# Performance work log

Measured on AMD Instinct MI355X. Metric: run time of the kernel, lower is better.

The kernel has to match this reference:

```python
import jax, jax.numpy as jnp
import numpy as np

N_NODES = 10000
N_EDGES = 320000
IN_FEATS = 512
N_UNITS = 256
OUT_FEATS = 64
N_LAYERS = 6  # number of hidden GCNConv layers feeding the JK max


def setup_inputs() -> dict:
    key = jax.random.key(0)
    ks = jax.random.split(key, 8)
    h = jax.random.normal(ks[0], (N_NODES, IN_FEATS), dtype=jnp.float32)
    edge_index = jax.random.randint(ks[1], (2, N_EDGES), 0, N_NODES, dtype=jnp.int64)
    # learned parameters (glorot-ish scale)
    W0 = jax.random.normal(ks[2], (IN_FEATS, N_UNITS), dtype=jnp.float32) * (1.0 / np.sqrt(IN_FEATS))
    b0 = jnp.zeros((N_UNITS,), dtype=jnp.float32)
    Wh = jax.random.normal(ks[3], (N_LAYERS - 1, N_UNITS, N_UNITS), dtype=jnp.float32) * (1.0 / np.sqrt(N_UNITS))
    bh = jnp.zeros((N_LAYERS - 1, N_UNITS), dtype=jnp.float32)
    Wo = jax.random.normal(ks[4], (N_UNITS, OUT_FEATS), dtype=jnp.float32) * (1.0 / np.sqrt(N_UNITS))
    bo = jnp.zeros((OUT_FEATS,), dtype=jnp.float32)
    return {"h": h, "edge_index": edge_index, "W0": W0, "b0": b0,
            "Wh": Wh, "bh": bh, "Wo": Wo, "bo": bo}


def reference(h, edge_index, W0, b0, Wh, bh, Wo, bo):
    src = edge_index[0]
    dst = edge_index[1]
    n = h.shape[0]

    def conv_plain(x, W, b):
        # GCNConv with normalize=False: plain sum aggregation over edges, no self-loops
        m = x @ W                                   # [N, d]
        agg = jax.ops.segment_sum(m[src], dst, num_segments=n)
        return jax.nn.relu(agg + b)

    outs = []
    x = conv_plain(h, W0, b0)
    outs.append(x)
    for i in range(Wh.shape[0]):  # dropout is identity in eval mode
        x = conv_plain(x, Wh[i], bh[i])
        outs.append(x)

    # jumping-knowledge max aggregation over layer outputs
    x = jnp.max(jnp.stack(outs, axis=0), axis=0)    # [N, n_units]

    # final GCNConv with normalize=True (symmetric GCN norm, self-loops added)
    m = x @ Wo                                      # [N, out_feats]
    ones = jnp.ones(dst.shape, dtype=m.dtype)
    deg = jax.ops.segment_sum(ones, dst, num_segments=n) + 1.0  # +1 self loop
    dinv = deg ** -0.5
    coef = dinv[src] * dinv[dst]                    # [E]
    agg = jax.ops.segment_sum(m[src] * coef[:, None], dst, num_segments=n)
    agg = agg + m / deg[:, None] + bo               # self-loop term 1/deg_i
    return jax.nn.log_softmax(agg, axis=-1)
```

## Files before the change

### kernel.cpp

```cpp
#include <hip/hip_runtime.h>
#include <math.h>

#define N_NODES 10000
#define N_EDGES 320000
#define IN_FEATS 512
#define N_UNITS 256
#define OUT_FEATS 64
#define N_HID 5

typedef __attribute__((ext_vector_type(8))) short bf16x8;
typedef __attribute__((ext_vector_type(4))) float f32x4;

__device__ __forceinline__ unsigned short f2bf(float f) {
    union { float f; unsigned int u; } c; c.f = f;
    unsigned int u = c.u + 0x7FFFu + ((c.u >> 16) & 1u);
    return (unsigned short)(u >> 16);
}
__device__ __forceinline__ float bf2f(unsigned int b) {
    union { unsigned int u; float f; } c; c.u = (b & 0xffffu) << 16;
    return c.f;
}


__global__ void k_setup(const int* __restrict__ dst, int* __restrict__ deg,
                        const float* __restrict__ h, unsigned short* __restrict__ hb,
                        const float* __restrict__ W0, const float* __restrict__ Wh,
                        const float* __restrict__ Wo,
                        unsigned short* __restrict__ W0t, unsigned short* __restrict__ Wht,
                        unsigned short* __restrict__ Wot) {
    const int R1 = N_EDGES;
    const int R2 = N_NODES * IN_FEATS / 4;
    const int S0 = IN_FEATS * N_UNITS;
    const int SH = N_HID * N_UNITS * N_UNITS;
    const int SO = N_UNITS * OUT_FEATS;
    int t = blockIdx.x * blockDim.x + threadIdx.x;
    if (t < R1) {
        atomicAdd(&deg[dst[t]], 1);
    } else if (t < R1 + R2) {
        int u = t - R1;
        float4 v = reinterpret_cast<const float4*>(h)[u];
        ushort4 o;
        o.x = f2bf(v.x); o.y = f2bf(v.y); o.z = f2bf(v.z); o.w = f2bf(v.w);
        reinterpret_cast<ushort4*>(hb)[u] = o;
    } else {
        int u = t - R1 - R2;
        if (u < S0) {
            int k = u >> 8, n = u & 255;
            W0t[(size_t)n * IN_FEATS + k] = f2bf(W0[u]);
        } else if (u < S0 + SH) {
            int w = u - S0;
            int l = w >> 16;
            int r = w & 65535;
            int k = r >> 8, n = r & 255;
            Wht[(size_t)l * 65536 + (size_t)n * N_UNITS + k] = f2bf(Wh[w]);
        } else if (u < S0 + SH + SO) {
            int w = u - S0 - SH;
            int k = w >> 6, n = w & 63;
            Wot[(size_t)n * N_UNITS + k] = f2bf(Wo[w]);
        }
    }
}


__global__ __launch_bounds__(1024) void k_scan(const int* __restrict__ deg,
                                               int* __restrict__ row_ptr,
                                               int* __restrict__ cursor,
                                               float* __restrict__ dinv,
                                               float* __restrict__ invdeg) {
    __shared__ int wsum[16];
    const int PER = 10;
    int t = threadIdx.x;
    int lane = t & 63, wid = t >> 6;
    int base = t * PER;

    int v[PER];
    int s = 0;
#pragma unroll
    for (int j = 0; j < PER; ++j) {
        int i = base + j;
        int d = (i < N_NODES) ? deg[i] : 0;
        v[j] = s;
        s += d;
    }
    int inc = s;
#pragma unroll
    for (int off = 1; off < 64; off <<= 1) {
        int y = __shfl_up(inc, off);
        if (lane >= off) inc += y;
    }
    if (lane == 63) wsum[wid] = inc;
    __syncthreads();
    if (wid == 0) {
        int w = (lane < 16) ? wsum[lane] : 0;
#pragma unroll
        for (int off = 1; off < 16; off <<= 1) {
            int y = __shfl_up(w, off);
            if (lane >= off) w += y;
        }
        if (lane < 16) wsum[lane] = w;
    }
    __syncthreads();
    int wave_excl = (wid == 0) ? 0 : wsum[wid - 1];
    int thread_excl = wave_excl + (inc - s);

#pragma unroll
    for (int j = 0; j < PER; ++j) {
        int i = base + j;
        if (i < N_NODES) {
            int rp = thread_excl + v[j];
            row_ptr[i] = rp;
            cursor[i]  = rp;
            int d = ((j + 1 < PER) ? v[j + 1] : s) - v[j];
            float dd = (float)(d + 1);
            dinv[i]   = rsqrtf(dd);
            invdeg[i] = 1.0f / dd;
        }
    }
    if (t == 1023) row_ptr[N_NODES] = thread_excl + s;
}

__global__ void k_fill(const int* __restrict__ src, const int* __restrict__ dst,
                       int* __restrict__ cursor, int* __restrict__ csr_src) {
    int e = blockIdx.x * blockDim.x + threadIdx.x;
    if (e < N_EDGES) {
        int p = atomicAdd(&cursor[dst[e]], 1);
        csr_src[p] = src[e];
    }
}


__global__ __launch_bounds__(256) void k_mgemm(const unsigned short* __restrict__ A,
                                               const unsigned short* __restrict__ Bt,
                                               unsigned short* __restrict__ C,
                                               const int M, const int K, const int Nld) {
    constexpr int BM = 64, BN = 64, BK = 32;
    __shared__ unsigned short As[2][BM * BK];
    __shared__ unsigned short Bs[2][BN * BK];

    const int tid  = threadIdx.x;
    const int wid  = tid >> 6;
    const int lane = tid & 63;
    const int wr   = wid >> 1;
    const int wc   = wid & 1;
    const int brow = blockIdx.x * BM;
    const int bcol = blockIdx.y * BN;

    const int lr = lane & 15;
    const int lk = lane >> 4;

    const int row  = tid >> 2;
    const int slot = tid & 3;
    const int sslot = slot ^ ((row >> 1) & 3);

    int gra = brow + row; if (gra >= M) gra = M - 1;
    const unsigned short* gpa = A + (size_t)gra * K + sslot * 8;
    const unsigned short* gpb = Bt + (size_t)(bcol + row) * K + sslot * 8;

    f32x4 acc[2][2];
#pragma unroll
    for (int m = 0; m < 2; ++m)
#pragma unroll
        for (int n = 0; n < 2; ++n)
            acc[m][n] = (f32x4){0.f, 0.f, 0.f, 0.f};

#define STAGE(buf, k0)                                                                      \
    do {                                                                                    \
        __builtin_amdgcn_global_load_lds(                                                   \
            (const __attribute__((address_space(1))) void*)(gpa + (k0)),                    \
            (__attribute__((address_space(3))) void*)(&As[(buf)][tid * 8]), 16, 0, 0);      \
        __builtin_amdgcn_global_load_lds(                                                   \
            (const __attribute__((address_space(1))) void*)(gpb + (k0)),                    \
            (__attribute__((address_space(3))) void*)(&Bs[(buf)][tid * 8]), 16, 0, 0);      \
    } while (0)

    STAGE(0, 0);
    __syncthreads();

    const int nk = K / BK;
    for (int kt = 0; kt < nk; ++kt) {
        const int cur = kt & 1;
        if (kt + 1 < nk) STAGE(cur ^ 1, (kt + 1) * BK);

        bf16x8 af[2], bfr[2];
#pragma unroll
        for (int m = 0; m < 2; ++m) {
            int ra = wr * 32 + m * 16 + lr;
            af[m] = *reinterpret_cast<const bf16x8*>(&As[cur][ra * BK + (lk ^ ((ra >> 1) & 3)) * 8]);
        }
#pragma unroll
        for (int n = 0; n < 2; ++n) {
            int rb = wc * 32 + n * 16 + lr;
            bfr[n] = *reinterpret_cast<const bf16x8*>(&Bs[cur][rb * BK + (lk ^ ((rb >> 1) & 3)) * 8]);
        }
#pragma unroll
        for (int m = 0; m < 2; ++m)
#pragma unroll
            for (int n = 0; n < 2; ++n)
                acc[m][n] = __builtin_amdgcn_mfma_f32_16x16x32_bf16(af[m], bfr[n], acc[m][n], 0, 0, 0);
        __syncthreads();
    }
#undef STAGE

#pragma unroll
    for (int m = 0; m < 2; ++m) {
#pragma unroll
        for (int r = 0; r < 4; ++r) {
            int orow = brow + wr * 32 + m * 16 + lk * 4 + r;
            if (orow < M) {
#pragma unroll
                for (int n = 0; n < 2; ++n) {
                    int ocol = bcol + wc * 32 + n * 16 + lr;
                    C[(size_t)orow * Nld + ocol] = f2bf(acc[m][n][r]);
                }
            }
        }
    }
}


__global__ __launch_bounds__(256) void k_wgemm(const unsigned short* __restrict__ A,
                                               const unsigned short* __restrict__ Bt,
                                               unsigned short* __restrict__ C,
                                               const int M, const int Nld) {
    constexpr int K = 256;
    __shared__ unsigned short As[64 * K];
    __shared__ unsigned short Bs[64 * K];

    const int tid  = threadIdx.x;
    const int wid  = tid >> 6;
    const int lane = tid & 63;
    const int lr   = lane & 15;
    const int lk   = lane >> 4;
    const int brow = blockIdx.x * 64;
    const int bcol = blockIdx.y * 64;

#pragma unroll
    for (int p = 0; p < 8; ++p) {
        int i = p * 256 + tid;
        int row = i >> 5, s = i & 31;
        int gr = brow + row; if (gr >= M) gr = M - 1;
        const unsigned short* gp = A + (size_t)gr * K + ((s ^ (row & 7)) * 8);
        __builtin_amdgcn_global_load_lds(
            (const __attribute__((address_space(1))) void*)gp,
            (__attribute__((address_space(3))) void*)(As + i * 8), 16, 0, 0);
    }
#pragma unroll
    for (int p = 0; p < 8; ++p) {
        int i = p * 256 + tid;
        int row = i >> 5, s = i & 31;
        const unsigned short* gp = Bt + (size_t)(bcol + row) * K + ((s ^ (row & 7)) * 8);
        __builtin_amdgcn_global_load_lds(
            (const __attribute__((address_space(1))) void*)gp,
            (__attribute__((address_space(3))) void*)(Bs + i * 8), 16, 0, 0);
    }
    __syncthreads();

    f32x4 acc[4];
#pragma unroll
    for (int n = 0; n < 4; ++n) acc[n] = (f32x4){0.f, 0.f, 0.f, 0.f};

    const int ra = (wid << 4) + lr;
    const unsigned short* Arow = As + ra * K;
    const int e = lr & 7;
#pragma unroll
    for (int kk = 0; kk < 8; ++kk) {
        bf16x8 av = *reinterpret_cast<const bf16x8*>(&Arow[(((kk << 2) + lk) ^ e) * 8]);
#pragma unroll
        for (int n = 0; n < 4; ++n) {
            const unsigned short* Brow = Bs + ((n << 4) + lr) * K;
            bf16x8 bv = *reinterpret_cast<const bf16x8*>(&Brow[(((kk << 2) + lk) ^ e) * 8]);
            acc[n] = __builtin_amdgcn_mfma_f32_16x16x32_bf16(av, bv, acc[n], 0, 0, 0);
        }
    }

#pragma unroll
    for (int n = 0; n < 4; ++n) {
#pragma unroll
        for (int r = 0; r < 4; ++r) {
            int orow = brow + (wid << 4) + (lk << 2) + r;
            if (orow < M) {
                int ocol = bcol + (n << 4) + lr;
                C[(size_t)orow * Nld + ocol] = f2bf(acc[n][r]);
            }
        }
    }
}


__global__ __launch_bounds__(256) void k_agg(const unsigned short* __restrict__ m,
                                             const int* __restrict__ row_ptr,
                                             const int* __restrict__ csr_src,
                                             const float* __restrict__ bias,
                                             unsigned short* __restrict__ x_out,
                                             unsigned short* __restrict__ jk,
                                             int init_jk) {
    int half = threadIdx.x >> 5;
    int lane = threadIdx.x & 31;
    int n = blockIdx.x * 8 + half;
    int s = row_ptr[n], e = row_ptr[n + 1];
    const uint4* mv = (const uint4*)m;

    float a[8];
#pragma unroll
    for (int j = 0; j < 8; ++j) a[j] = 0.f;

#define ACC8(u)                                        \
    do {                                               \
        a[0] += bf2f((u).x); a[1] += bf2f((u).x >> 16);\
        a[2] += bf2f((u).y); a[3] += bf2f((u).y >> 16);\
        a[4] += bf2f((u).z); a[5] += bf2f((u).z >> 16);\
        a[6] += bf2f((u).w); a[7] += bf2f((u).w >> 16);\
    } while (0)

    int i = s;
    for (; i + 3 < e; i += 4) {
        int s0 = csr_src[i], s1 = csr_src[i + 1], s2 = csr_src[i + 2], s3 = csr_src[i + 3];
        uint4 u0 = mv[(size_t)s0 * 32 + lane];
        uint4 u1 = mv[(size_t)s1 * 32 + lane];
        uint4 u2 = mv[(size_t)s2 * 32 + lane];
        uint4 u3 = mv[(size_t)s3 * 32 + lane];
        ACC8(u0); ACC8(u1); ACC8(u2); ACC8(u3);
    }
    for (; i < e; ++i) {
        uint4 u = mv[(size_t)csr_src[i] * 32 + lane];
        ACC8(u);
    }
#undef ACC8

    float4 b0 = ((const float4*)bias)[lane * 2];
    float4 b1 = ((const float4*)bias)[lane * 2 + 1];
    unsigned int hh[8];
    hh[0] = f2bf(fmaxf(a[0] + b0.x, 0.f));
    hh[1] = f2bf(fmaxf(a[1] + b0.y, 0.f));
    hh[2] = f2bf(fmaxf(a[2] + b0.z, 0.f));
    hh[3] = f2bf(fmaxf(a[3] + b0.w, 0.f));
    hh[4] = f2bf(fmaxf(a[4] + b1.x, 0.f));
    hh[5] = f2bf(fmaxf(a[5] + b1.y, 0.f));
    hh[6] = f2bf(fmaxf(a[6] + b1.z, 0.f));
    hh[7] = f2bf(fmaxf(a[7] + b1.w, 0.f));
    uint4 o;
    o.x = hh[0] | (hh[1] << 16);
    o.y = hh[2] | (hh[3] << 16);
    o.z = hh[4] | (hh[5] << 16);
    o.w = hh[6] | (hh[7] << 16);

    size_t idx = (size_t)n * 32 + lane;
    ((uint4*)x_out)[idx] = o;
    if (init_jk) {
        ((uint4*)jk)[idx] = o;
    } else {
        uint4 j = ((const uint4*)jk)[idx];
        auto mx2 = [](unsigned int nw, unsigned int od) {
            unsigned int lo_n = nw & 0xffffu, lo_o = od & 0xffffu;
            unsigned int hi_n = nw >> 16,     hi_o = od >> 16;
            unsigned int lo = lo_n > lo_o ? lo_n : lo_o;
            unsigned int hi = hi_n > hi_o ? hi_n : hi_o;
            return lo | (hi << 16);
        };
        uint4 w;
        w.x = mx2(o.x, j.x); w.y = mx2(o.y, j.y);
        w.z = mx2(o.z, j.z); w.w = mx2(o.w, j.w);
        ((uint4*)jk)[idx] = w;
    }
}


__global__ __launch_bounds__(256) void k_final(const unsigned short* __restrict__ mf,
                                               const int* __restrict__ row_ptr,
                                               const int* __restrict__ csr_src,
                                               const float* __restrict__ dinv,
                                               const float* __restrict__ invdeg,
                                               const float* __restrict__ bo,
                                               float* __restrict__ out) {
    int wid  = threadIdx.x >> 6;
    int lane = threadIdx.x & 63;
    int n = blockIdx.x * 4 + wid;
    if (n >= N_NODES) return;

    int s = row_ptr[n], e = row_ptr[n + 1];
    float acc = 0.f;
    int i = s;
    for (; i + 3 < e; i += 4) {
        int s0 = csr_src[i], s1 = csr_src[i + 1], s2 = csr_src[i + 2], s3 = csr_src[i + 3];
        acc += bf2f(mf[(size_t)s0 * OUT_FEATS + lane]) * dinv[s0];
        acc += bf2f(mf[(size_t)s1 * OUT_FEATS + lane]) * dinv[s1];
        acc += bf2f(mf[(size_t)s2 * OUT_FEATS + lane]) * dinv[s2];
        acc += bf2f(mf[(size_t)s3 * OUT_FEATS + lane]) * dinv[s3];
    }
    for (; i < e; ++i) {
        int sr = csr_src[i];
        acc += bf2f(mf[(size_t)sr * OUT_FEATS + lane]) * dinv[sr];
    }
    acc *= dinv[n];
    acc += bf2f(mf[(size_t)n * OUT_FEATS + lane]) * invdeg[n] + bo[lane];

    float mx = acc;
#pragma unroll
    for (int off = 32; off; off >>= 1) mx = fmaxf(mx, __shfl_xor(mx, off));
    float ex = __expf(acc - mx);
    float sum = ex;
#pragma unroll
    for (int off = 32; off; off >>= 1) sum += __shfl_xor(sum, off);
    out[(size_t)n * OUT_FEATS + lane] = acc - mx - __logf(sum);
}


extern "C" void kernel_launch(void* const* d_in, const int* in_sizes, int n_in,
                              void* d_out, int out_size, void* d_ws, size_t ws_size,
                              hipStream_t stream) {
    const float* h  = (const float*)d_in[0];
    const int*   ei = (const int*)d_in[1];
    const float* W0 = (const float*)d_in[2];
    const float* b0 = (const float*)d_in[3];
    const float* Wh = (const float*)d_in[4];
    const float* bh = (const float*)d_in[5];
    const float* Wo = (const float*)d_in[6];
    const float* bo = (const float*)d_in[7];

    const int* src = ei;
    const int* dst = ei + N_EDGES;

    char* p = (char*)d_ws;
    auto carve = [&](size_t bytes) {
        char* r = p;
        p += (bytes + 255) & ~(size_t)255;
        return r;
    };
    int*   deg     = (int*)  carve(N_NODES * 4);
    int*   row_ptr = (int*)  carve((N_NODES + 1) * 4);
    int*   cursor  = (int*)  carve(N_NODES * 4);
    int*   csr_src = (int*)  carve(N_EDGES * 4);
    float* dinv    = (float*)carve(N_NODES * 4);
    float* invdeg  = (float*)carve(N_NODES * 4);
    unsigned short* hb  = (unsigned short*)carve((size_t)N_NODES * IN_FEATS * 2);
    unsigned short* W0t = (unsigned short*)carve((size_t)IN_FEATS * N_UNITS * 2);
    unsigned short* Wht = (unsigned short*)carve((size_t)N_HID * N_UNITS * N_UNITS * 2);
    unsigned short* Wot = (unsigned short*)carve((size_t)N_UNITS * OUT_FEATS * 2);
    unsigned short* m   = (unsigned short*)carve((size_t)N_NODES * N_UNITS * 2);
    unsigned short* x   = (unsigned short*)carve((size_t)N_NODES * N_UNITS * 2);
    unsigned short* jk  = (unsigned short*)carve((size_t)N_NODES * N_UNITS * 2);
    unsigned short* mf  = (unsigned short*)carve((size_t)N_NODES * OUT_FEATS * 2);

    hipMemsetAsync(deg, 0, N_NODES * 4, stream);
    {
        const int total = N_EDGES + N_NODES * IN_FEATS / 4 +
                          IN_FEATS * N_UNITS + N_HID * N_UNITS * N_UNITS + N_UNITS * OUT_FEATS;
        k_setup<<<(total + 255) / 256, 256, 0, stream>>>(dst, deg, h, hb, W0, Wh, Wo,
                                                         W0t, Wht, Wot);
    }
    k_scan<<<1, 1024, 0, stream>>>(deg, row_ptr, cursor, dinv, invdeg);
    k_fill<<<(N_EDGES + 255) / 256, 256, 0, stream>>>(src, dst, cursor, csr_src);

    const int GBM = (N_NODES + 63) / 64;

    {
        dim3 g(GBM, N_UNITS / 64);
        k_mgemm<<<g, 256, 0, stream>>>(hb, W0t, m, N_NODES, IN_FEATS, N_UNITS);
    }
    k_agg<<<N_NODES / 8, 256, 0, stream>>>(m, row_ptr, csr_src, b0, x, jk, 1);

    for (int l = 0; l < N_HID; ++l) {
        dim3 g(GBM, N_UNITS / 64);
        k_wgemm<<<g, 256, 0, stream>>>(x, Wht + (size_t)l * N_UNITS * N_UNITS, m,
                                       N_NODES, N_UNITS);
        k_agg<<<N_NODES / 8, 256, 0, stream>>>(m, row_ptr, csr_src, bh + (size_t)l * N_UNITS,
                                               x, jk, 0);
    }

    {
        dim3 g(GBM, 1);
        k_wgemm<<<g, 256, 0, stream>>>(jk, Wot, mf, N_NODES, OUT_FEATS);
    }
    k_final<<<(N_NODES + 3) / 4, 256, 0, stream>>>(mf, row_ptr, csr_src, dinv, invdeg,
                                                   bo, (float*)d_out);
}
```

Before: 258.1 us.

## Fuse hidden-layer aggregation and GEMM by aggregating before the weight multiply

Hidden layers now compute (A·x)·W instead of A·(x·W). A single fused kernel gathers neighbor rows of x into LDS, then multiplies by the weight tile with MFMA and applies bias, ReLU and the JK max in the epilogue. This drops the separate GEMM launch and the round trip through the intermediate m buffer, and uses ping-pong x buffers. It adds a bf16 rounding of the aggregated sum before the GEMM and uses scalar 2-byte epilogue stores and jk reads. The final kernel is also reworked to use half-waves with packed bf16 pairs, handling 8 nodes per block.

```diff
diff --git a/kernel.cpp b/kernel.cpp
--- a/kernel.cpp
+++ b/kernel.cpp
@@ -49,8 +49,7 @@
             W0t[(size_t)n * IN_FEATS + k] = f2bf(W0[u]);
         } else if (u < S0 + SH) {
             int w = u - S0;
-            int l = w >> 16;
-            int r = w & 65535;
+            int l = w >> 16, r = w & 65535;
             int k = r >> 8, n = r & 255;
             Wht[(size_t)l * 65536 + (size_t)n * N_UNITS + k] = f2bf(Wh[w]);
         } else if (u < S0 + SH + SO) {
@@ -218,82 +217,12 @@
 }
 
 
-__global__ __launch_bounds__(256) void k_wgemm(const unsigned short* __restrict__ A,
-                                               const unsigned short* __restrict__ Bt,
-                                               unsigned short* __restrict__ C,
-                                               const int M, const int Nld) {
-    constexpr int K = 256;
-    __shared__ unsigned short As[64 * K];
-    __shared__ unsigned short Bs[64 * K];
-
-    const int tid  = threadIdx.x;
-    const int wid  = tid >> 6;
-    const int lane = tid & 63;
-    const int lr   = lane & 15;
-    const int lk   = lane >> 4;
-    const int brow = blockIdx.x * 64;
-    const int bcol = blockIdx.y * 64;
-
-#pragma unroll
-    for (int p = 0; p < 8; ++p) {
-        int i = p * 256 + tid;
-        int row = i >> 5, s = i & 31;
-        int gr = brow + row; if (gr >= M) gr = M - 1;
-        const unsigned short* gp = A + (size_t)gr * K + ((s ^ (row & 7)) * 8);
-        __builtin_amdgcn_global_load_lds(
-            (const __attribute__((address_space(1))) void*)gp,
-            (__attribute__((address_space(3))) void*)(As + i * 8), 16, 0, 0);
-    }
-#pragma unroll
-    for (int p = 0; p < 8; ++p) {
-        int i = p * 256 + tid;
-        int row = i >> 5, s = i & 31;
-        const unsigned short* gp = Bt + (size_t)(bcol + row) * K + ((s ^ (row & 7)) * 8);
-        __builtin_amdgcn_global_load_lds(
-            (const __attribute__((address_space(1))) void*)gp,
-            (__attribute__((address_space(3))) void*)(Bs + i * 8), 16, 0, 0);
-    }
-    __syncthreads();
-
-    f32x4 acc[4];
-#pragma unroll
-    for (int n = 0; n < 4; ++n) acc[n] = (f32x4){0.f, 0.f, 0.f, 0.f};
-
-    const int ra = (wid << 4) + lr;
-    const unsigned short* Arow = As + ra * K;
-    const int e = lr & 7;
-#pragma unroll
-    for (int kk = 0; kk < 8; ++kk) {
-        bf16x8 av = *reinterpret_cast<const bf16x8*>(&Arow[(((kk << 2) + lk) ^ e) * 8]);
-#pragma unroll
-        for (int n = 0; n < 4; ++n) {
-            const unsigned short* Brow = Bs + ((n << 4) + lr) * K;
-            bf16x8 bv = *reinterpret_cast<const bf16x8*>(&Brow[(((kk << 2) + lk) ^ e) * 8]);
-            acc[n] = __builtin_amdgcn_mfma_f32_16x16x32_bf16(av, bv, acc[n], 0, 0, 0);
-        }
-    }
-
-#pragma unroll
-    for (int n = 0; n < 4; ++n) {
-#pragma unroll
-        for (int r = 0; r < 4; ++r) {
-            int orow = brow + (wid << 4) + (lk << 2) + r;
-            if (orow < M) {
-                int ocol = bcol + (n << 4) + lr;
-                C[(size_t)orow * Nld + ocol] = f2bf(acc[n][r]);
-            }
-        }
-    }
-}
-
-
-__global__ __launch_bounds__(256) void k_agg(const unsigned short* __restrict__ m,
-                                             const int* __restrict__ row_ptr,
-                                             const int* __restrict__ csr_src,
-                                             const float* __restrict__ bias,
-                                             unsigned short* __restrict__ x_out,
-                                             unsigned short* __restrict__ jk,
-                                             int init_jk) {
+__global__ __launch_bounds__(256) void k_agg0(const unsigned short* __restrict__ m,
+                                              const int* __restrict__ row_ptr,
+                                              const int* __restrict__ csr_src,
+                                              const float* __restrict__ bias,
+                                              unsigned short* __restrict__ x_out,
+                                              unsigned short* __restrict__ jk) {
     int half = threadIdx.x >> 5;
     int lane = threadIdx.x & 31;
     int n = blockIdx.x * 8 + half;
@@ -346,21 +275,191 @@
 
     size_t idx = (size_t)n * 32 + lane;
     ((uint4*)x_out)[idx] = o;
-    if (init_jk) {
-        ((uint4*)jk)[idx] = o;
-    } else {
-        uint4 j = ((const uint4*)jk)[idx];
-        auto mx2 = [](unsigned int nw, unsigned int od) {
-            unsigned int lo_n = nw & 0xffffu, lo_o = od & 0xffffu;
-            unsigned int hi_n = nw >> 16,     hi_o = od >> 16;
-            unsigned int lo = lo_n > lo_o ? lo_n : lo_o;
-            unsigned int hi = hi_n > hi_o ? hi_n : hi_o;
-            return lo | (hi << 16);
-        };
-        uint4 w;
-        w.x = mx2(o.x, j.x); w.y = mx2(o.y, j.y);
-        w.z = mx2(o.z, j.z); w.w = mx2(o.w, j.w);
-        ((uint4*)jk)[idx] = w;
+    ((uint4*)jk)[idx] = o;
+}
+
+
+__global__ __launch_bounds__(256) void k_fused(const unsigned short* __restrict__ x_in,
+                                               const int* __restrict__ row_ptr,
+                                               const int* __restrict__ csr_src,
+                                               const unsigned short* __restrict__ Bt,
+                                               const float* __restrict__ bias,
+                                               unsigned short* __restrict__ x_out,
+                                               unsigned short* __restrict__ jk) {
+    constexpr int K = 256;
+    __shared__ unsigned short U[64 * K];
+    __shared__ unsigned short Bs[64 * K];
+
+    const int tid = threadIdx.x;
+    const int brow = blockIdx.x * 64;
+    const uint4* xv = (const uint4*)x_in;
+
+    {
+        const int hw = tid >> 5;
+        const int hl = tid & 31;
+        for (int j = 0; j < 8; ++j) {
+            int r = hw * 8 + j;
+            int n = brow + r;
+            float a[8];
+#pragma unroll
+            for (int q = 0; q < 8; ++q) a[q] = 0.f;
+
+            if (n < N_NODES) {
+                int s = row_ptr[n], e = row_ptr[n + 1];
+#define ACC8(u)                                        \
+    do {                                               \
+        a[0] += bf2f((u).x); a[1] += bf2f((u).x >> 16);\
+        a[2] += bf2f((u).y); a[3] += bf2f((u).y >> 16);\
+        a[4] += bf2f((u).z); a[5] += bf2f((u).z >> 16);\
+        a[6] += bf2f((u).w); a[7] += bf2f((u).w >> 16);\
+    } while (0)
+                int i = s;
+                for (; i + 7 < e; i += 8) {
+                    uint4 u0 = xv[(size_t)csr_src[i + 0] * 32 + hl];
+                    uint4 u1 = xv[(size_t)csr_src[i + 1] * 32 + hl];
+                    uint4 u2 = xv[(size_t)csr_src[i + 2] * 32 + hl];
+                    uint4 u3 = xv[(size_t)csr_src[i + 3] * 32 + hl];
+                    uint4 u4 = xv[(size_t)csr_src[i + 4] * 32 + hl];
+                    uint4 u5 = xv[(size_t)csr_src[i + 5] * 32 + hl];
+                    uint4 u6 = xv[(size_t)csr_src[i + 6] * 32 + hl];
+                    uint4 u7 = xv[(size_t)csr_src[i + 7] * 32 + hl];
+                    ACC8(u0); ACC8(u1); ACC8(u2); ACC8(u3);
+                    ACC8(u4); ACC8(u5); ACC8(u6); ACC8(u7);
+                }
+                for (; i < e; ++i) {
+                    uint4 u = xv[(size_t)csr_src[i] * 32 + hl];
+                    ACC8(u);
+                }
+#undef ACC8
+            }
+            unsigned int p0 = f2bf(a[0]) | ((unsigned int)f2bf(a[1]) << 16);
+            unsigned int p1 = f2bf(a[2]) | ((unsigned int)f2bf(a[3]) << 16);
+            unsigned int p2 = f2bf(a[4]) | ((unsigned int)f2bf(a[5]) << 16);
+            unsigned int p3 = f2bf(a[6]) | ((unsigned int)f2bf(a[7]) << 16);
+            uint4 o; o.x = p0; o.y = p1; o.z = p2; o.w = p3;
+            ((uint4*)U)[r * 32 + (hl ^ (r & 7))] = o;
+        }
+    }
+    __syncthreads();
+
+    const int wid = tid >> 6, lane = tid & 63;
+    const int lr = lane & 15, lk = lane >> 4;
+    const unsigned short* Urow = U + (wid * 16 + lr) * K;
+    const int e8 = lr & 7;
+
+    for (int ct = 0; ct < 4; ++ct) {
+#pragma unroll
+        for (int p = 0; p < 8; ++p) {
+            int i = p * 256 + tid;
+            int row = i >> 5, s = i & 31;
+            const unsigned short* gp = Bt + (size_t)(ct * 64 + row) * K + ((s ^ (row & 7)) * 8);
+            __builtin_amdgcn_global_load_lds(
+                (const __attribute__((address_space(1))) void*)gp,
+                (__attribute__((address_space(3))) void*)(Bs + i * 8), 16, 0, 0);
+        }
+        __syncthreads();
+
+        f32x4 acc[4];
+#pragma unroll
+        for (int n = 0; n < 4; ++n) acc[n] = (f32x4){0.f, 0.f, 0.f, 0.f};
+
+#pragma unroll
+        for (int kk = 0; kk < 8; ++kk) {
+            bf16x8 av = *reinterpret_cast<const bf16x8*>(&Urow[(((kk << 2) + lk) ^ e8) * 8]);
+#pragma unroll
+            for (int n = 0; n < 4; ++n) {
+                const unsigned short* Brow = Bs + ((n << 4) + lr) * K;
+                bf16x8 bv = *reinterpret_cast<const bf16x8*>(&Brow[(((kk << 2) + lk) ^ e8) * 8]);
+                acc[n] = __builtin_amdgcn_mfma_f32_16x16x32_bf16(av, bv, acc[n], 0, 0, 0);
+            }
+        }
+
+#pragma unroll
+        for (int n = 0; n < 4; ++n) {
+            int col = ct * 64 + (n << 4) + lr;
+            float bv = bias[col];
+#pragma unroll
+            for (int rr = 0; rr < 4; ++rr) {
+                int orow = brow + wid * 16 + (lk << 2) + rr;
+                if (orow < N_NODES) {
+                    unsigned short xb = f2bf(fmaxf(acc[n][rr] + bv, 0.f));
+                    size_t idx = (size_t)orow * N_UNITS + col;
+                    x_out[idx] = xb;
+                    unsigned short jb = jk[idx];
+                    jk[idx] = (xb > jb) ? xb : jb;
+                }
+            }
+        }
+        __syncthreads();
+    }
+}
+
+
+__global__ __launch_bounds__(256) void k_wgemm(const unsigned short* __restrict__ A,
+                                               const unsigned short* __restrict__ Bt,
+                                               unsigned short* __restrict__ C,
+                                               const int M, const int Nld) {
+    constexpr int K = 256;
+    __shared__ unsigned short As[64 * K];
+    __shared__ unsigned short Bs[64 * K];
+
+    const int tid  = threadIdx.x;
+    const int wid  = tid >> 6;
+    const int lane = tid & 63;
+    const int lr   = lane & 15;
+    const int lk   = lane >> 4;
+    const int brow = blockIdx.x * 64;
+    const int bcol = blockIdx.y * 64;
+
+#pragma unroll
+    for (int p = 0; p < 8; ++p) {
+        int i = p * 256 + tid;
+        int row = i >> 5, s = i & 31;
+        int gr = brow + row; if (gr >= M) gr = M - 1;
+        const unsigned short* gp = A + (size_t)gr * K + ((s ^ (row & 7)) * 8);
+        __builtin_amdgcn_global_load_lds(
+            (const __attribute__((address_space(1))) void*)gp,
+            (__attribute__((address_space(3))) void*)(As + i * 8), 16, 0, 0);
+    }
+#pragma unroll
+    for (int p = 0; p < 8; ++p) {
+        int i = p * 256 + tid;
+        int row = i >> 5, s = i & 31;
+        const unsigned short* gp = Bt + (size_t)(bcol + row) * K + ((s ^ (row & 7)) * 8);
+        __builtin_amdgcn_global_load_lds(
+            (const __attribute__((address_space(1))) void*)gp,
+            (__attribute__((address_space(3))) void*)(Bs + i * 8), 16, 0, 0);
+    }
+    __syncthreads();
+
+    f32x4 acc[4];
+#pragma unroll
+    for (int n = 0; n < 4; ++n) acc[n] = (f32x4){0.f, 0.f, 0.f, 0.f};
+
+    const int ra = (wid << 4) + lr;
+    const unsigned short* Arow = As + ra * K;
+    const int e = lr & 7;
+#pragma unroll
+    for (int kk = 0; kk < 8; ++kk) {
+        bf16x8 av = *reinterpret_cast<const bf16x8*>(&Arow[(((kk << 2) + lk) ^ e) * 8]);
+#pragma unroll
+        for (int n = 0; n < 4; ++n) {
+            const unsigned short* Brow = Bs + ((n << 4) + lr) * K;
+            bf16x8 bv = *reinterpret_cast<const bf16x8*>(&Brow[(((kk << 2) + lk) ^ e) * 8]);
+            acc[n] = __builtin_amdgcn_mfma_f32_16x16x32_bf16(av, bv, acc[n], 0, 0, 0);
+        }
+    }
+
+#pragma unroll
+    for (int n = 0; n < 4; ++n) {
+#pragma unroll
+        for (int r = 0; r < 4; ++r) {
+            int orow = brow + (wid << 4) + (lk << 2) + r;
+            if (orow < M) {
+                int ocol = bcol + (n << 4) + lr;
+                C[(size_t)orow * Nld + ocol] = f2bf(acc[n][r]);
+            }
+        }
     }
 }
 
@@ -372,36 +471,49 @@
                                                const float* __restrict__ invdeg,
                                                const float* __restrict__ bo,
                                                float* __restrict__ out) {
-    int wid  = threadIdx.x >> 6;
-    int lane = threadIdx.x & 63;
-    int n = blockIdx.x * 4 + wid;
-    if (n >= N_NODES) return;
-
+    int halfw = threadIdx.x >> 5;
+    int wl = threadIdx.x & 31;
+    const unsigned int* mfu = (const unsigned int*)mf;
+    int n = blockIdx.x * 8 + halfw;
     int s = row_ptr[n], e = row_ptr[n + 1];
-    float acc = 0.f;
+
+    float a0 = 0.f, a1 = 0.f;
     int i = s;
-    for (; i + 3 < e; i += 4) {
-        int s0 = csr_src[i], s1 = csr_src[i + 1], s2 = csr_src[i + 2], s3 = csr_src[i + 3];
-        acc += bf2f(mf[(size_t)s0 * OUT_FEATS + lane]) * dinv[s0];
-        acc += bf2f(mf[(size_t)s1 * OUT_FEATS + lane]) * dinv[s1];
-        acc += bf2f(mf[(size_t)s2 * OUT_FEATS + lane]) * dinv[s2];
-        acc += bf2f(mf[(size_t)s3 * OUT_FEATS + lane]) * dinv[s3];
+    for (; i + 1 < e; i += 2) {
+        int s0 = csr_src[i], s1 = csr_src[i + 1];
+        unsigned int u0 = mfu[(size_t)s0 * 32 + wl];
+        unsigned int u1 = mfu[(size_t)s1 * 32 + wl];
+        float d0 = dinv[s0], d1 = dinv[s1];
+        a0 += bf2f(u0) * d0 + bf2f(u1) * d1;
+        a1 += bf2f(u0 >> 16) * d0 + bf2f(u1 >> 16) * d1;
     }
     for (; i < e; ++i) {
         int sr = csr_src[i];
-        acc += bf2f(mf[(size_t)sr * OUT_FEATS + lane]) * dinv[sr];
-    }
-    acc *= dinv[n];
-    acc += bf2f(mf[(size_t)n * OUT_FEATS + lane]) * invdeg[n] + bo[lane];
-
-    float mx = acc;
-#pragma unroll
-    for (int off = 32; off; off >>= 1) mx = fmaxf(mx, __shfl_xor(mx, off));
-    float ex = __expf(acc - mx);
-    float sum = ex;
-#pragma unroll
-    for (int off = 32; off; off >>= 1) sum += __shfl_xor(sum, off);
-    out[(size_t)n * OUT_FEATS + lane] = acc - mx - __logf(sum);
+        unsigned int u = mfu[(size_t)sr * 32 + wl];
+        float dv = dinv[sr];
+        a0 += bf2f(u) * dv;
+        a1 += bf2f(u >> 16) * dv;
+    }
+    float dn = dinv[n];
+    a0 *= dn; a1 *= dn;
+    unsigned int un = mfu[(size_t)n * 32 + wl];
+    float idg = invdeg[n];
+    float2 bo2 = ((const float2*)bo)[wl];
+    a0 += bf2f(un) * idg + bo2.x;
+    a1 += bf2f(un >> 16) * idg + bo2.y;
+
+    float mx = fmaxf(a0, a1);
+#pragma unroll
+    for (int off = 16; off; off >>= 1) mx = fmaxf(mx, __shfl_xor(mx, off));
+    float e0 = __expf(a0 - mx), e1 = __expf(a1 - mx);
+    float sum = e0 + e1;
+#pragma unroll
+    for (int off = 16; off; off >>= 1) sum += __shfl_xor(sum, off);
+    float ls = __logf(sum);
+    float2 r;
+    r.x = a0 - mx - ls;
+    r.y = a1 - mx - ls;
+    ((float2*)out)[(size_t)n * 32 + wl] = r;
 }
 
 
@@ -437,7 +549,8 @@
     unsigned short* Wht = (unsigned short*)carve((size_t)N_HID * N_UNITS * N_UNITS * 2);
     unsigned short* Wot = (unsigned short*)carve((size_t)N_UNITS * OUT_FEATS * 2);
     unsigned short* m   = (unsigned short*)carve((size_t)N_NODES * N_UNITS * 2);
-    unsigned short* x   = (unsigned short*)carve((size_t)N_NODES * N_UNITS * 2);
+    unsigned short* xa  = (unsigned short*)carve((size_t)N_NODES * N_UNITS * 2);
+    unsigned short* xb  = (unsigned short*)carve((size_t)N_NODES * N_UNITS * 2);
     unsigned short* jk  = (unsigned short*)carve((size_t)N_NODES * N_UNITS * 2);
     unsigned short* mf  = (unsigned short*)carve((size_t)N_NODES * OUT_FEATS * 2);
 
@@ -457,20 +570,21 @@
         dim3 g(GBM, N_UNITS / 64);
         k_mgemm<<<g, 256, 0, stream>>>(hb, W0t, m, N_NODES, IN_FEATS, N_UNITS);
     }
-    k_agg<<<N_NODES / 8, 256, 0, stream>>>(m, row_ptr, csr_src, b0, x, jk, 1);
-
+    k_agg0<<<N_NODES / 8, 256, 0, stream>>>(m, row_ptr, csr_src, b0, xa, jk);
+
+    unsigned short* cur = xa;
+    unsigned short* nxt = xb;
     for (int l = 0; l < N_HID; ++l) {
-        dim3 g(GBM, N_UNITS / 64);
-        k_wgemm<<<g, 256, 0, stream>>>(x, Wht + (size_t)l * N_UNITS * N_UNITS, m,
-                                       N_NODES, N_UNITS);
-        k_agg<<<N_NODES / 8, 256, 0, stream>>>(m, row_ptr, csr_src, bh + (size_t)l * N_UNITS,
-                                               x, jk, 0);
+        k_fused<<<GBM, 256, 0, stream>>>(cur, row_ptr, csr_src,
+                                         Wht + (size_t)l * N_UNITS * N_UNITS,
+                                         bh + (size_t)l * N_UNITS, nxt, jk);
+        unsigned short* t = cur; cur = nxt; nxt = t;
     }
 
     {
         dim3 g(GBM, 1);
         k_wgemm<<<g, 256, 0, stream>>>(jk, Wot, mf, N_NODES, OUT_FEATS);
     }
-    k_final<<<(N_NODES + 3) / 4, 256, 0, stream>>>(mf, row_ptr, csr_src, dinv, invdeg,
-                                                   bo, (float*)d_out);
-}
+    k_final<<<N_NODES / 8, 256, 0, stream>>>(mf, row_ptr, csr_src, dinv, invdeg,
+                                             bo, (float*)d_out);
+}
```

Result: slower. 452.3 us (+75.2%).

## Swap GEMM grid order, split aggregation by feature half, halve final-layer lanes

Applied to the files above, without the earlier changes.

The GEMM grids are transposed so consecutive blocks cover column tiles of the same row block, which should let them share the A tile in cache. The aggregation kernel now gives each node 16 lanes per 128-feature half, run as two grid halves. Each half then gathers only 256 bytes per neighbour row, aiming for better L2 locality of the feature slice. The final normalized conv uses 32 lanes per node with packed bf16 pairs and float2 stores, cutting thread count and shuffle steps, though each thread now does more gather work.

```diff
diff --git a/kernel.cpp b/kernel.cpp
--- a/kernel.cpp
+++ b/kernel.cpp
@@ -49,8 +49,7 @@
             W0t[(size_t)n * IN_FEATS + k] = f2bf(W0[u]);
         } else if (u < S0 + SH) {
             int w = u - S0;
-            int l = w >> 16;
-            int r = w & 65535;
+            int l = w >> 16, r = w & 65535;
             int k = r >> 8, n = r & 255;
             Wht[(size_t)l * 65536 + (size_t)n * N_UNITS + k] = f2bf(Wh[w]);
         } else if (u < S0 + SH + SO) {
@@ -142,8 +141,8 @@
     const int lane = tid & 63;
     const int wr   = wid >> 1;
     const int wc   = wid & 1;
-    const int brow = blockIdx.x * BM;
-    const int bcol = blockIdx.y * BN;
+    const int brow = blockIdx.y * BM;
+    const int bcol = blockIdx.x * BN;
 
     const int lr = lane & 15;
     const int lk = lane >> 4;
@@ -231,8 +230,8 @@
     const int lane = tid & 63;
     const int lr   = lane & 15;
     const int lk   = lane >> 4;
-    const int brow = blockIdx.x * 64;
-    const int bcol = blockIdx.y * 64;
+    const int brow = blockIdx.y * 64;
+    const int bcol = blockIdx.x * 64;
 
 #pragma unroll
     for (int p = 0; p < 8; ++p) {
@@ -294,11 +293,14 @@
                                              unsigned short* __restrict__ x_out,
                                              unsigned short* __restrict__ jk,
                                              int init_jk) {
-    int half = threadIdx.x >> 5;
-    int lane = threadIdx.x & 31;
-    int n = blockIdx.x * 8 + half;
-    int s = row_ptr[n], e = row_ptr[n + 1];
+    const int halfsel = (blockIdx.x >= 625) ? 1 : 0;
+    const int g = blockIdx.x - halfsel * 625;
+    const int nib  = threadIdx.x >> 4;
+    const int lane = threadIdx.x & 15;
+    const int n = g * 16 + nib;
+    const int s = row_ptr[n], e = row_ptr[n + 1];
     const uint4* mv = (const uint4*)m;
+    const int off = halfsel * 16 + lane;
 
     float a[8];
 #pragma unroll
@@ -315,20 +317,20 @@
     int i = s;
     for (; i + 3 < e; i += 4) {
         int s0 = csr_src[i], s1 = csr_src[i + 1], s2 = csr_src[i + 2], s3 = csr_src[i + 3];
-        uint4 u0 = mv[(size_t)s0 * 32 + lane];
-        uint4 u1 = mv[(size_t)s1 * 32 + lane];
-        uint4 u2 = mv[(size_t)s2 * 32 + lane];
-        uint4 u3 = mv[(size_t)s3 * 32 + lane];
+        uint4 u0 = mv[(size_t)s0 * 32 + off];
+        uint4 u1 = mv[(size_t)s1 * 32 + off];
+        uint4 u2 = mv[(size_t)s2 * 32 + off];
+        uint4 u3 = mv[(size_t)s3 * 32 + off];
         ACC8(u0); ACC8(u1); ACC8(u2); ACC8(u3);
     }
     for (; i < e; ++i) {
-        uint4 u = mv[(size_t)csr_src[i] * 32 + lane];
+        uint4 u = mv[(size_t)csr_src[i] * 32 + off];
         ACC8(u);
     }
 #undef ACC8
 
-    float4 b0 = ((const float4*)bias)[lane * 2];
-    float4 b1 = ((const float4*)bias)[lane * 2 + 1];
+    float4 b0 = ((const float4*)bias)[halfsel * 32 + lane * 2];
+    float4 b1 = ((const float4*)bias)[halfsel * 32 + lane * 2 + 1];
     unsigned int hh[8];
     hh[0] = f2bf(fmaxf(a[0] + b0.x, 0.f));
     hh[1] = f2bf(fmaxf(a[1] + b0.y, 0.f));
@@ -344,7 +346,7 @@
     o.z = hh[4] | (hh[5] << 16);
     o.w = hh[6] | (hh[7] << 16);
 
-    size_t idx = (size_t)n * 32 + lane;
+    size_t idx = (size_t)n * 32 + off;
     ((uint4*)x_out)[idx] = o;
     if (init_jk) {
         ((uint4*)jk)[idx] = o;
@@ -372,36 +374,49 @@
                                                const float* __restrict__ invdeg,
                                                const float* __restrict__ bo,
                                                float* __restrict__ out) {
-    int wid  = threadIdx.x >> 6;
-    int lane = threadIdx.x & 63;
-    int n = blockIdx.x * 4 + wid;
-    if (n >= N_NODES) return;
-
+    int halfw = threadIdx.x >> 5;
+    int wl = threadIdx.x & 31;
+    const unsigned int* mfu = (const unsigned int*)mf;
+    int n = blockIdx.x * 8 + halfw;
     int s = row_ptr[n], e = row_ptr[n + 1];
-    float acc = 0.f;
+
+    float a0 = 0.f, a1 = 0.f;
     int i = s;
-    for (; i + 3 < e; i += 4) {
-        int s0 = csr_src[i], s1 = csr_src[i + 1], s2 = csr_src[i + 2], s3 = csr_src[i + 3];
-        acc += bf2f(mf[(size_t)s0 * OUT_FEATS + lane]) * dinv[s0];
-        acc += bf2f(mf[(size_t)s1 * OUT_FEATS + lane]) * dinv[s1];
-        acc += bf2f(mf[(size_t)s2 * OUT_FEATS + lane]) * dinv[s2];
-        acc += bf2f(mf[(size_t)s3 * OUT_FEATS + lane]) * dinv[s3];
+    for (; i + 1 < e; i += 2) {
+        int s0 = csr_src[i], s1 = csr_src[i + 1];
+        unsigned int u0 = mfu[(size_t)s0 * 32 + wl];
+        unsigned int u1 = mfu[(size_t)s1 * 32 + wl];
+        float d0 = dinv[s0], d1 = dinv[s1];
+        a0 += bf2f(u0) * d0 + bf2f(u1) * d1;
+        a1 += bf2f(u0 >> 16) * d0 + bf2f(u1 >> 16) * d1;
     }
     for (; i < e; ++i) {
         int sr = csr_src[i];
-        acc += bf2f(mf[(size_t)sr * OUT_FEATS + lane]) * dinv[sr];
-    }
-    acc *= dinv[n];
-    acc += bf2f(mf[(size_t)n * OUT_FEATS + lane]) * invdeg[n] + bo[lane];
-
-    float mx = acc;
-#pragma unroll
-    for (int off = 32; off; off >>= 1) mx = fmaxf(mx, __shfl_xor(mx, off));
-    float ex = __expf(acc - mx);
-    float sum = ex;
-#pragma unroll
-    for (int off = 32; off; off >>= 1) sum += __shfl_xor(sum, off);
-    out[(size_t)n * OUT_FEATS + lane] = acc - mx - __logf(sum);
+        unsigned int u = mfu[(size_t)sr * 32 + wl];
+        float dv = dinv[sr];
+        a0 += bf2f(u) * dv;
+        a1 += bf2f(u >> 16) * dv;
+    }
+    float dn = dinv[n];
+    a0 *= dn; a1 *= dn;
+    unsigned int un = mfu[(size_t)n * 32 + wl];
+    float idg = invdeg[n];
+    float2 bo2 = ((const float2*)bo)[wl];
+    a0 += bf2f(un) * idg + bo2.x;
+    a1 += bf2f(un >> 16) * idg + bo2.y;
+
+    float mx = fmaxf(a0, a1);
+#pragma unroll
+    for (int off = 16; off; off >>= 1) mx = fmaxf(mx, __shfl_xor(mx, off));
+    float e0 = __expf(a0 - mx), e1 = __expf(a1 - mx);
+    float sum = e0 + e1;
+#pragma unroll
+    for (int off = 16; off; off >>= 1) sum += __shfl_xor(sum, off);
+    float ls = __logf(sum);
+    float2 r;
+    r.x = a0 - mx - ls;
+    r.y = a1 - mx - ls;
+    ((float2*)out)[(size_t)n * 32 + wl] = r;
 }
 
 
@@ -454,23 +469,23 @@
     const int GBM = (N_NODES + 63) / 64;
 
     {
-        dim3 g(GBM, N_UNITS / 64);
+        dim3 g(N_UNITS / 64, GBM);
         k_mgemm<<<g, 256, 0, stream>>>(hb, W0t, m, N_NODES, IN_FEATS, N_UNITS);
     }
-    k_agg<<<N_NODES / 8, 256, 0, stream>>>(m, row_ptr, csr_src, b0, x, jk, 1);
+    k_agg<<<1250, 256, 0, stream>>>(m, row_ptr, csr_src, b0, x, jk, 1);
 
     for (int l = 0; l < N_HID; ++l) {
-        dim3 g(GBM, N_UNITS / 64);
+        dim3 g(N_UNITS / 64, GBM);
         k_wgemm<<<g, 256, 0, stream>>>(x, Wht + (size_t)l * N_UNITS * N_UNITS, m,
                                        N_NODES, N_UNITS);
-        k_agg<<<N_NODES / 8, 256, 0, stream>>>(m, row_ptr, csr_src, bh + (size_t)l * N_UNITS,
-                                               x, jk, 0);
+        k_agg<<<1250, 256, 0, stream>>>(m, row_ptr, csr_src, bh + (size_t)l * N_UNITS,
+                                        x, jk, 0);
     }
 
     {
-        dim3 g(GBM, 1);
+        dim3 g(OUT_FEATS / 64, GBM);
         k_wgemm<<<g, 256, 0, stream>>>(jk, Wot, mf, N_NODES, OUT_FEATS);
     }
-    k_final<<<(N_NODES + 3) / 4, 256, 0, stream>>>(mf, row_ptr, csr_src, dinv, invdeg,
-                                                   bo, (float*)d_out);
-}
+    k_final<<<N_NODES / 8, 256, 0, stream>>>(mf, row_ptr, csr_src, dinv, invdeg,
+                                             bo, (float*)d_out);
+}
```

Measured after the change: 262.6 us. Within noise of the previous version (+1.7%).
